# Optimization experiments

Hardware: AMD Instinct MI355X
Metric: run time of the kernel (lower is better)

## Reference

```python
import jax, jax.numpy as jnp
import numpy as np

B, NB, F, N = 8192, 64, 256, 1_000_000
K = 8            # per-channel top-k
KS = K // 2 + 1  # conv1d kernel size = 5
H, OUT = 256, 128
DN = ('NWC', 'WIO', 'NWC')


def setup_inputs() -> dict:
    key = jax.random.key(0)
    ks = jax.random.split(key, 7)
    return {
        'node_ids': jax.random.randint(ks[0], (B,), 0, N, dtype=jnp.int64) if jax.config.jax_enable_x64 else jax.random.randint(ks[0], (B,), 0, N, dtype=jnp.int32),
        'neighbors': jax.random.randint(ks[1], (B, NB), 0, N, dtype=jnp.int32),
        'feat_table': jax.random.normal(ks[2], (N, F), dtype=jnp.float32),
        'W1': jax.random.normal(ks[3], (KS, F, H), dtype=jnp.float32) * 0.05,
        'b1': jnp.zeros((H,), dtype=jnp.float32),
        'W2': jax.random.normal(ks[4], (KS, H, OUT), dtype=jnp.float32) * 0.05,
        'b2': jnp.zeros((OUT,), dtype=jnp.float32),
    }


def reference(node_ids, neighbors, feat_table, W1, b1, W2, b2):
    node_feats = feat_table[node_ids][:, None, :]          # [B, 1, F]
    nb_feats = feat_table[neighbors]                       # [B, NB, F] irregular gather
    # per-channel top-k over neighbors
    topk, _ = jax.lax.top_k(jnp.transpose(nb_feats, (0, 2, 1)), K)  # [B, F, K]
    topk = jnp.transpose(topk, (0, 2, 1))                  # [B, K, F]
    x = jnp.concatenate([node_feats, topk], axis=1)        # [B, K+1, F]
    h = jax.lax.conv_general_dilated(x, W1, (1,), 'VALID', dimension_numbers=DN) + b1  # [B, K+2-KS, H]
    o = jax.lax.conv_general_dilated(h, W2, (1,), 'VALID', dimension_numbers=DN) + b2  # [B, 1, OUT]
    return o[:, 0, :]                                      # [B, OUT]
```

## Files before the change

### kernel.cpp

```cpp
#include <hip/hip_runtime.h>
#include <hip/hip_bf16.h>

namespace {
constexpr int kB    = 8192;
constexpr int kNB   = 64;
constexpr int kF    = 256;
constexpr int kK    = 8;
constexpr int kKS   = 5;
constexpr int kH    = 256;
constexpr int kOUT  = 128;
constexpr int kXR   = 9;
constexpr int kTO   = 5;
constexpr int kBM   = 16;

constexpr int XPAD = 258;
constexpr int HPAD = 1290;

constexpr int DEPTH = 12;

constexpr size_t W1T_OFF = 0;
constexpr size_t W2T_OFF = W1T_OFF + (size_t)kKS * kH * kF * 2;

typedef __attribute__((ext_vector_type(8))) short short8;
typedef __attribute__((ext_vector_type(4))) float f32x4;
}

using bf16 = __hip_bfloat16;

__device__ __forceinline__ unsigned short f2bf(float f) {
  bf16 h = __float2bfloat16(f);
  return *reinterpret_cast<unsigned short*>(&h);
}

__device__ __forceinline__ f32x4 nt_load4(const float* p) {
  return __builtin_nontemporal_load(reinterpret_cast<const f32x4*>(p));
}

__global__ void convert_weights(const float* __restrict__ W1,
                                const float* __restrict__ W2,
                                bf16* __restrict__ w1t, bf16* __restrict__ w2t)
{
  const int i = blockIdx.x * 256 + threadIdx.x;
  const int stride = gridDim.x * 256;
  for (int idx = i; idx < kKS * kH * kF; idx += stride) {
    const int f  = idx & 255;
    const int hc = (idx >> 8) & 255;
    const int dt = idx >> 16;
    w1t[idx] = __float2bfloat16(W1[(dt * kF + f) * kH + hc]);
  }
  for (int idx = i; idx < kOUT * kKS * kH; idx += stride) {
    const int k = idx % (kKS * kH);
    const int o = idx / (kKS * kH);
    w2t[idx] = __float2bfloat16(W2[k * kOUT + o]);
  }
}

__global__ __launch_bounds__(512, 4)
void fused_all(const int* __restrict__ node_ids,
               const int* __restrict__ neighbors,
               const float* __restrict__ feat,
               const bf16* __restrict__ w1t, const bf16* __restrict__ w2t,
               const float* __restrict__ b1, const float* __restrict__ b2,
               float* __restrict__ out)
{
  __shared__ bf16 smem[kBM * kXR * XPAD];
  bf16* xs = smem;
  bf16* hs = smem;

  const int tid  = threadIdx.x;
  const int wave = tid >> 6;
  const int lane = tid & 63;
  const int r = lane & 15;
  const int q = lane >> 4;
  const int bbase = blockIdx.x * kBM;
  const int f4 = lane << 2;

  int   myn2[2];
  f32x4 node2[2];
#pragma unroll
  for (int bb = 0; bb < 2; ++bb) {
    const int b = bbase + wave * 2 + bb;
    myn2[bb]  = neighbors[(size_t)b * kNB + lane];
    node2[bb] = nt_load4(feat + (size_t)node_ids[b] * kF + f4);
  }

#pragma unroll
  for (int bb = 0; bb < 2; ++bb) {
    const int bl  = wave * 2 + bb;
    const int myn = myn2[bb];

    float tk[4][kK];
#pragma unroll
    for (int c = 0; c < 4; ++c)
#pragma unroll
      for (int k = 0; k < kK; ++k) tk[c][k] = -INFINITY;

    auto ins4 = [&](const f32x4& v) {
#pragma unroll
      for (int c = 0; c < 4; ++c) {
        const float vc = v[c];
        float nt[kK];
        nt[0] = fmaxf(tk[c][0], vc);
#pragma unroll
        for (int k = 1; k < kK; ++k)
          nt[k] = __builtin_amdgcn_fmed3f(tk[c][k - 1], tk[c][k], vc);
#pragma unroll
        for (int k = 0; k < kK; ++k) tk[c][k] = nt[k];
      }
    };

    f32x4 buf[DEPTH];
#pragma unroll
    for (int i = 0; i < DEPTH; ++i) {
      const int rr = __builtin_amdgcn_readlane(myn, i);
      buf[i] = nt_load4(feat + (size_t)rr * kF + f4);
    }
#pragma unroll
    for (int n = 0; n < kNB - DEPTH; ++n) {
      const f32x4 v = buf[n % DEPTH];
      const int rr = __builtin_amdgcn_readlane(myn, n + DEPTH);
      buf[n % DEPTH] = nt_load4(feat + (size_t)rr * kF + f4);
      ins4(v);
    }
#pragma unroll
    for (int n = kNB - DEPTH; n < kNB; ++n) ins4(buf[n % DEPTH]);

    bf16* xb = xs + (size_t)bl * kXR * XPAD + f4;
    {
      ushort4 s = {f2bf(node2[bb][0]), f2bf(node2[bb][1]),
                   f2bf(node2[bb][2]), f2bf(node2[bb][3])};
      *reinterpret_cast<ushort4*>(xb) = s;
    }
#pragma unroll
    for (int k = 0; k < kK; ++k) {
      ushort4 s = {f2bf(tk[0][k]), f2bf(tk[1][k]), f2bf(tk[2][k]), f2bf(tk[3][k])};
      *reinterpret_cast<ushort4*>(xb + (size_t)(1 + k) * XPAD) = s;
    }
  }
  __syncthreads();

  const int ntb = wave * 32;
  f32x4 acc[kTO][2];
#pragma unroll
  for (int n = 0; n < 2; ++n) {
    const float bv = b1[ntb + n * 16 + r];
#pragma unroll
    for (int m = 0; m < kTO; ++m) acc[m][n] = (f32x4){bv, bv, bv, bv};
  }

  for (int kk = 0; kk < 8; ++kk) {
    short8 a[kXR];
#pragma unroll
    for (int rr = 0; rr < kXR; ++rr)
      a[rr] = *reinterpret_cast<const short8*>(&xs[(r * kXR + rr) * XPAD + kk * 32 + q * 8]);
#pragma unroll
    for (int dt = 0; dt < kKS; ++dt) {
      short8 bfr[2];
#pragma unroll
      for (int n = 0; n < 2; ++n)
        bfr[n] = *reinterpret_cast<const short8*>(
            &w1t[((size_t)(dt * kH + ntb + n * 16 + r)) * kF + kk * 32 + q * 8]);
#pragma unroll
      for (int m = 0; m < kTO; ++m)
#pragma unroll
        for (int n = 0; n < 2; ++n)
          acc[m][n] = __builtin_amdgcn_mfma_f32_16x16x32_bf16(a[m + dt], bfr[n], acc[m][n], 0, 0, 0);
    }
  }
  __syncthreads();

#pragma unroll
  for (int m = 0; m < kTO; ++m)
#pragma unroll
    for (int n = 0; n < 2; ++n)
#pragma unroll
      for (int j = 0; j < 4; ++j)
        hs[(q * 4 + j) * HPAD + m * kH + ntb + n * 16 + r] = __float2bfloat16(acc[m][n][j]);
  __syncthreads();

  const int ob = wave * 16;
  f32x4 acc2;
  {
    const float bv = b2[ob + r];
    acc2 = (f32x4){bv, bv, bv, bv};
  }
  for (int ks = 0; ks < 40; ++ks) {
    short8 a2 = *reinterpret_cast<const short8*>(&hs[r * HPAD + ks * 32 + q * 8]);
    short8 b2f = *reinterpret_cast<const short8*>(
        &w2t[(size_t)(ob + r) * (kKS * kH) + ks * 32 + q * 8]);
    acc2 = __builtin_amdgcn_mfma_f32_16x16x32_bf16(a2, b2f, acc2, 0, 0, 0);
  }
#pragma unroll
  for (int j = 0; j < 4; ++j)
    out[(size_t)(bbase + q * 4 + j) * kOUT + ob + r] = acc2[j];
}

extern "C" void kernel_launch(void* const* d_in, const int* in_sizes, int n_in,
                              void* d_out, int out_size, void* d_ws, size_t ws_size,
                              hipStream_t stream) {
  const int*   node_ids  = (const int*)  d_in[0];
  const int*   neighbors = (const int*)  d_in[1];
  const float* feat      = (const float*)d_in[2];
  const float* W1        = (const float*)d_in[3];
  const float* b1        = (const float*)d_in[4];
  const float* W2        = (const float*)d_in[5];
  const float* b2        = (const float*)d_in[6];
  float* out = (float*)d_out;

  char* ws = (char*)d_ws;
  bf16* w1t = (bf16*)(ws + W1T_OFF);
  bf16* w2t = (bf16*)(ws + W2T_OFF);

  convert_weights<<<1024, 256, 0, stream>>>(W1, W2, w1t, w2t);
  fused_all<<<kB / kBM, 512, 0, stream>>>(node_ids, neighbors, feat, w1t, w2t, b1, b2, out);
}
```

Baseline: 141.7 us.

## Double batch tile to 32 rows per block and drop nontemporal gather loads

```diff
diff --git a/kernel.cpp b/kernel.cpp
--- a/kernel.cpp
+++ b/kernel.cpp
@@ -11,7 +11,7 @@
 constexpr int kOUT  = 128;
 constexpr int kXR   = 9;
 constexpr int kTO   = 5;
-constexpr int kBM   = 16;
+constexpr int kBM   = 32;
 
 constexpr int XPAD = 258;
 constexpr int HPAD = 1290;
@@ -30,10 +30,6 @@
 __device__ __forceinline__ unsigned short f2bf(float f) {
   bf16 h = __float2bfloat16(f);
   return *reinterpret_cast<unsigned short*>(&h);
-}
-
-__device__ __forceinline__ f32x4 nt_load4(const float* p) {
-  return __builtin_nontemporal_load(reinterpret_cast<const f32x4*>(p));
 }
 
 __global__ void convert_weights(const float* __restrict__ W1,
@@ -55,7 +51,7 @@
   }
 }
 
-__global__ __launch_bounds__(512, 4)
+__global__ __launch_bounds__(512, 2)
 void fused_all(const int* __restrict__ node_ids,
                const int* __restrict__ neighbors,
                const float* __restrict__ feat,
@@ -75,19 +71,19 @@
   const int bbase = blockIdx.x * kBM;
   const int f4 = lane << 2;
 
-  int   myn2[2];
-  f32x4 node2[2];
-#pragma unroll
-  for (int bb = 0; bb < 2; ++bb) {
-    const int b = bbase + wave * 2 + bb;
-    myn2[bb]  = neighbors[(size_t)b * kNB + lane];
-    node2[bb] = nt_load4(feat + (size_t)node_ids[b] * kF + f4);
-  }
-
-#pragma unroll
-  for (int bb = 0; bb < 2; ++bb) {
-    const int bl  = wave * 2 + bb;
-    const int myn = myn2[bb];
+  int   myn4[4];
+  f32x4 node4[4];
+#pragma unroll
+  for (int bb = 0; bb < 4; ++bb) {
+    const int b = bbase + wave * 4 + bb;
+    myn4[bb]  = neighbors[(size_t)b * kNB + lane];
+    node4[bb] = *reinterpret_cast<const f32x4*>(feat + (size_t)node_ids[b] * kF + f4);
+  }
+
+#pragma unroll
+  for (int bb = 0; bb < 4; ++bb) {
+    const int bl  = wave * 4 + bb;
+    const int myn = myn4[bb];
 
     float tk[4][kK];
 #pragma unroll
@@ -113,13 +109,13 @@
 #pragma unroll
     for (int i = 0; i < DEPTH; ++i) {
       const int rr = __builtin_amdgcn_readlane(myn, i);
-      buf[i] = nt_load4(feat + (size_t)rr * kF + f4);
+      buf[i] = *reinterpret_cast<const f32x4*>(feat + (size_t)rr * kF + f4);
     }
 #pragma unroll
     for (int n = 0; n < kNB - DEPTH; ++n) {
       const f32x4 v = buf[n % DEPTH];
       const int rr = __builtin_amdgcn_readlane(myn, n + DEPTH);
-      buf[n % DEPTH] = nt_load4(feat + (size_t)rr * kF + f4);
+      buf[n % DEPTH] = *reinterpret_cast<const f32x4*>(feat + (size_t)rr * kF + f4);
       ins4(v);
     }
 #pragma unroll
@@ -127,8 +123,8 @@
 
     bf16* xb = xs + (size_t)bl * kXR * XPAD + f4;
     {
-      ushort4 s = {f2bf(node2[bb][0]), f2bf(node2[bb][1]),
-                   f2bf(node2[bb][2]), f2bf(node2[bb][3])};
+      ushort4 s = {f2bf(node4[bb][0]), f2bf(node4[bb][1]),
+                   f2bf(node4[bb][2]), f2bf(node4[bb][3])};
       *reinterpret_cast<ushort4*>(xb) = s;
     }
 #pragma unroll
@@ -140,19 +136,24 @@
   __syncthreads();
 
   const int ntb = wave * 32;
-  f32x4 acc[kTO][2];
+  f32x4 acc[2][kTO][2];
 #pragma unroll
   for (int n = 0; n < 2; ++n) {
     const float bv = b1[ntb + n * 16 + r];
 #pragma unroll
-    for (int m = 0; m < kTO; ++m) acc[m][n] = (f32x4){bv, bv, bv, bv};
+    for (int mt = 0; mt < 2; ++mt)
+#pragma unroll
+      for (int m = 0; m < kTO; ++m) acc[mt][m][n] = (f32x4){bv, bv, bv, bv};
   }
 
   for (int kk = 0; kk < 8; ++kk) {
-    short8 a[kXR];
-#pragma unroll
-    for (int rr = 0; rr < kXR; ++rr)
-      a[rr] = *reinterpret_cast<const short8*>(&xs[(r * kXR + rr) * XPAD + kk * 32 + q * 8]);
+    short8 a[2][kXR];
+#pragma unroll
+    for (int mt = 0; mt < 2; ++mt)
+#pragma unroll
+      for (int rr = 0; rr < kXR; ++rr)
+        a[mt][rr] = *reinterpret_cast<const short8*>(
+            &xs[((mt * 16 + r) * kXR + rr) * XPAD + kk * 32 + q * 8]);
 #pragma unroll
     for (int dt = 0; dt < kKS; ++dt) {
       short8 bfr[2];
@@ -161,38 +162,51 @@
         bfr[n] = *reinterpret_cast<const short8*>(
             &w1t[((size_t)(dt * kH + ntb + n * 16 + r)) * kF + kk * 32 + q * 8]);
 #pragma unroll
-      for (int m = 0; m < kTO; ++m)
-#pragma unroll
-        for (int n = 0; n < 2; ++n)
-          acc[m][n] = __builtin_amdgcn_mfma_f32_16x16x32_bf16(a[m + dt], bfr[n], acc[m][n], 0, 0, 0);
+      for (int mt = 0; mt < 2; ++mt)
+#pragma unroll
+        for (int m = 0; m < kTO; ++m)
+#pragma unroll
+          for (int n = 0; n < 2; ++n)
+            acc[mt][m][n] = __builtin_amdgcn_mfma_f32_16x16x32_bf16(
+                a[mt][m + dt], bfr[n], acc[mt][m][n], 0, 0, 0);
     }
   }
   __syncthreads();
 
 #pragma unroll
-  for (int m = 0; m < kTO; ++m)
-#pragma unroll
-    for (int n = 0; n < 2; ++n)
-#pragma unroll
-      for (int j = 0; j < 4; ++j)
-        hs[(q * 4 + j) * HPAD + m * kH + ntb + n * 16 + r] = __float2bfloat16(acc[m][n][j]);
+  for (int mt = 0; mt < 2; ++mt)
+#pragma unroll
+    for (int m = 0; m < kTO; ++m)
+#pragma unroll
+      for (int n = 0; n < 2; ++n)
+#pragma unroll
+        for (int j = 0; j < 4; ++j)
+          hs[(mt * 16 + q * 4 + j) * HPAD + m * kH + ntb + n * 16 + r] =
+              __float2bfloat16(acc[mt][m][n][j]);
   __syncthreads();
 
   const int ob = wave * 16;
-  f32x4 acc2;
+  f32x4 acc2[2];
   {
     const float bv = b2[ob + r];
-    acc2 = (f32x4){bv, bv, bv, bv};
+#pragma unroll
+    for (int mt = 0; mt < 2; ++mt) acc2[mt] = (f32x4){bv, bv, bv, bv};
   }
   for (int ks = 0; ks < 40; ++ks) {
-    short8 a2 = *reinterpret_cast<const short8*>(&hs[r * HPAD + ks * 32 + q * 8]);
     short8 b2f = *reinterpret_cast<const short8*>(
         &w2t[(size_t)(ob + r) * (kKS * kH) + ks * 32 + q * 8]);
-    acc2 = __builtin_amdgcn_mfma_f32_16x16x32_bf16(a2, b2f, acc2, 0, 0, 0);
-  }
-#pragma unroll
-  for (int j = 0; j < 4; ++j)
-    out[(size_t)(bbase + q * 4 + j) * kOUT + ob + r] = acc2[j];
+#pragma unroll
+    for (int mt = 0; mt < 2; ++mt) {
+      short8 a2 = *reinterpret_cast<const short8*>(
+          &hs[(mt * 16 + r) * HPAD + ks * 32 + q * 8]);
+      acc2[mt] = __builtin_amdgcn_mfma_f32_16x16x32_bf16(a2, b2f, acc2[mt], 0, 0, 0);
+    }
+  }
+#pragma unroll
+  for (int mt = 0; mt < 2; ++mt)
+#pragma unroll
+    for (int j = 0; j < 4; ++j)
+      out[(size_t)(bbase + mt * 16 + q * 4 + j) * kOUT + ob + r] = acc2[mt][j];
 }
 
 extern "C" void kernel_launch(void* const* d_in, const int* in_sizes, int n_in,
```

Result: no change. 144.5 us (+1.9%).

## Process two tiles per block, overlapping next tile's gather with current GEMMs

Applied to the files above, without the earlier changes.

```diff
diff --git a/kernel.cpp b/kernel.cpp
--- a/kernel.cpp
+++ b/kernel.cpp
@@ -12,11 +12,10 @@
 constexpr int kXR   = 9;
 constexpr int kTO   = 5;
 constexpr int kBM   = 16;
+constexpr int kTiles = 2;
 
 constexpr int XPAD = 258;
 constexpr int HPAD = 1290;
-
-constexpr int DEPTH = 12;
 
 constexpr size_t W1T_OFF = 0;
 constexpr size_t W2T_OFF = W1T_OFF + (size_t)kKS * kH * kF * 2;
@@ -32,8 +31,54 @@
   return *reinterpret_cast<unsigned short*>(&h);
 }
 
-__device__ __forceinline__ f32x4 nt_load4(const float* p) {
-  return __builtin_nontemporal_load(reinterpret_cast<const f32x4*>(p));
+__device__ __forceinline__ void ins4(const f32x4& v, float (&tk)[4][kK]) {
+#pragma unroll
+  for (int c = 0; c < 4; ++c) {
+    const float vc = v[c];
+    float nt[kK];
+    nt[0] = fmaxf(tk[c][0], vc);
+#pragma unroll
+    for (int k = 1; k < kK; ++k)
+      nt[k] = __builtin_amdgcn_fmed3f(tk[c][k - 1], tk[c][k], vc);
+#pragma unroll
+    for (int k = 0; k < kK; ++k) tk[c][k] = nt[k];
+  }
+}
+
+__device__ __forceinline__ f32x4 rowload(const float* feat, int myn, int idx, int f4) {
+  const unsigned rr = (unsigned)__builtin_amdgcn_readlane(myn, idx);
+  return *reinterpret_cast<const f32x4*>(feat + (size_t)rr * kF + f4);
+}
+
+__device__ __forceinline__ void store_x(bf16* xb, const f32x4& nodev, float (&tk)[4][kK]) {
+  ushort4 s0 = {f2bf(nodev[0]), f2bf(nodev[1]), f2bf(nodev[2]), f2bf(nodev[3])};
+  *reinterpret_cast<ushort4*>(xb) = s0;
+#pragma unroll
+  for (int k = 0; k < kK; ++k) {
+    ushort4 s = {f2bf(tk[0][k]), f2bf(tk[1][k]), f2bf(tk[2][k]), f2bf(tk[3][k])};
+    *reinterpret_cast<ushort4*>(xb + (size_t)(1 + k) * XPAD) = s;
+  }
+}
+
+__device__ __forceinline__ void gather_row(const float* feat, int myn, int f4,
+                                           const f32x4& nodev, bf16* xb) {
+  float tk[4][kK];
+#pragma unroll
+  for (int c = 0; c < 4; ++c)
+#pragma unroll
+    for (int k = 0; k < kK; ++k) tk[c][k] = -INFINITY;
+  f32x4 buf[8];
+#pragma unroll
+  for (int i = 0; i < 8; ++i) buf[i] = rowload(feat, myn, i, f4);
+#pragma unroll
+  for (int g = 0; g < 8; ++g)
+#pragma unroll
+    for (int i = 0; i < 8; ++i) {
+      const f32x4 v = buf[i];
+      if (g < 7) buf[i] = rowload(feat, myn, g * 8 + i + 8, f4);
+      ins4(v, tk);
+    }
+  store_x(xb, nodev, tk);
 }
 
 __global__ void convert_weights(const float* __restrict__ W1,
@@ -55,7 +100,7 @@
   }
 }
 
-__global__ __launch_bounds__(512, 4)
+__global__ __launch_bounds__(512, 2)
 void fused_all(const int* __restrict__ node_ids,
                const int* __restrict__ neighbors,
                const float* __restrict__ feat,
@@ -63,83 +108,53 @@
                const float* __restrict__ b1, const float* __restrict__ b2,
                float* __restrict__ out)
 {
-  __shared__ bf16 smem[kBM * kXR * XPAD];
-  bf16* xs = smem;
-  bf16* hs = smem;
+  __shared__ bf16 smem[2 * kBM * kXR * XPAD];
+  bf16* xsA = smem;
+  bf16* xsB = smem + (size_t)kBM * kXR * XPAD;
+  bf16* hs  = smem;
 
   const int tid  = threadIdx.x;
   const int wave = tid >> 6;
   const int lane = tid & 63;
   const int r = lane & 15;
   const int q = lane >> 4;
-  const int bbase = blockIdx.x * kBM;
   const int f4 = lane << 2;
 
-  int   myn2[2];
-  f32x4 node2[2];
-#pragma unroll
-  for (int bb = 0; bb < 2; ++bb) {
-    const int b = bbase + wave * 2 + bb;
-    myn2[bb]  = neighbors[(size_t)b * kNB + lane];
-    node2[bb] = nt_load4(feat + (size_t)node_ids[b] * kF + f4);
-  }
-
-#pragma unroll
-  for (int bb = 0; bb < 2; ++bb) {
-    const int bl  = wave * 2 + bb;
-    const int myn = myn2[bb];
-
-    float tk[4][kK];
-#pragma unroll
-    for (int c = 0; c < 4; ++c)
-#pragma unroll
-      for (int k = 0; k < kK; ++k) tk[c][k] = -INFINITY;
-
-    auto ins4 = [&](const f32x4& v) {
-#pragma unroll
-      for (int c = 0; c < 4; ++c) {
-        const float vc = v[c];
-        float nt[kK];
-        nt[0] = fmaxf(tk[c][0], vc);
-#pragma unroll
-        for (int k = 1; k < kK; ++k)
-          nt[k] = __builtin_amdgcn_fmed3f(tk[c][k - 1], tk[c][k], vc);
-#pragma unroll
-        for (int k = 0; k < kK; ++k) tk[c][k] = nt[k];
-      }
-    };
-
-    f32x4 buf[DEPTH];
-#pragma unroll
-    for (int i = 0; i < DEPTH; ++i) {
-      const int rr = __builtin_amdgcn_readlane(myn, i);
-      buf[i] = nt_load4(feat + (size_t)rr * kF + f4);
-    }
-#pragma unroll
-    for (int n = 0; n < kNB - DEPTH; ++n) {
-      const f32x4 v = buf[n % DEPTH];
-      const int rr = __builtin_amdgcn_readlane(myn, n + DEPTH);
-      buf[n % DEPTH] = nt_load4(feat + (size_t)rr * kF + f4);
-      ins4(v);
-    }
-#pragma unroll
-    for (int n = kNB - DEPTH; n < kNB; ++n) ins4(buf[n % DEPTH]);
-
-    bf16* xb = xs + (size_t)bl * kXR * XPAD + f4;
-    {
-      ushort4 s = {f2bf(node2[bb][0]), f2bf(node2[bb][1]),
-                   f2bf(node2[bb][2]), f2bf(node2[bb][3])};
-      *reinterpret_cast<ushort4*>(xb) = s;
-    }
-#pragma unroll
-    for (int k = 0; k < kK; ++k) {
-      ushort4 s = {f2bf(tk[0][k]), f2bf(tk[1][k]), f2bf(tk[2][k]), f2bf(tk[3][k])};
-      *reinterpret_cast<ushort4*>(xb + (size_t)(1 + k) * XPAD) = s;
-    }
-  }
-  __syncthreads();
+  const int tile0 = blockIdx.x;
+  const int tile1 = blockIdx.x + 256;
+  const int bbase0 = tile0 * kBM;
+  const int bbase1 = tile1 * kBM;
+
+  {
+    int   mynA[2];
+    f32x4 nodeA[2];
+#pragma unroll
+    for (int bb = 0; bb < 2; ++bb) {
+      const int b = bbase0 + wave * 2 + bb;
+      mynA[bb]  = neighbors[(size_t)b * kNB + lane];
+      nodeA[bb] = *reinterpret_cast<const f32x4*>(feat + (size_t)node_ids[b] * kF + f4);
+    }
+#pragma unroll
+    for (int bb = 0; bb < 2; ++bb)
+      gather_row(feat, mynA[bb], f4, nodeA[bb],
+                 xsA + (size_t)(wave * 2 + bb) * kXR * XPAD + f4);
+  }
+  __syncthreads();
+
+  int   mynB0, mynB1;
+  f32x4 nodeB0, nodeB1;
+  {
+    const int b0 = bbase1 + wave * 2 + 0;
+    const int b1r = bbase1 + wave * 2 + 1;
+    mynB0  = neighbors[(size_t)b0 * kNB + lane];
+    mynB1  = neighbors[(size_t)b1r * kNB + lane];
+    nodeB0 = *reinterpret_cast<const f32x4*>(feat + (size_t)node_ids[b0] * kF + f4);
+    nodeB1 = *reinterpret_cast<const f32x4*>(feat + (size_t)node_ids[b1r] * kF + f4);
+  }
 
   const int ntb = wave * 32;
+  const int ob  = wave * 16;
+
   f32x4 acc[kTO][2];
 #pragma unroll
   for (int n = 0; n < 2; ++n) {
@@ -148,11 +163,103 @@
     for (int m = 0; m < kTO; ++m) acc[m][n] = (f32x4){bv, bv, bv, bv};
   }
 
+  {
+    float tkB[4][kK];
+#pragma unroll
+    for (int c = 0; c < 4; ++c)
+#pragma unroll
+      for (int k = 0; k < kK; ++k) tkB[c][k] = -INFINITY;
+    f32x4 bufB[8];
+#pragma unroll
+    for (int i = 0; i < 8; ++i) bufB[i] = rowload(feat, mynB0, i, f4);
+
+    for (int kk = 0; kk < 8; ++kk) {
+#pragma unroll
+      for (int i = 0; i < 8; ++i) {
+        const f32x4 v = bufB[i];
+        if (kk < 7) bufB[i] = rowload(feat, mynB0, kk * 8 + i + 8, f4);
+        ins4(v, tkB);
+      }
+      short8 a[kXR];
+#pragma unroll
+      for (int rr = 0; rr < kXR; ++rr)
+        a[rr] = *reinterpret_cast<const short8*>(&xsA[(r * kXR + rr) * XPAD + kk * 32 + q * 8]);
+#pragma unroll
+      for (int dt = 0; dt < kKS; ++dt) {
+        short8 bfr[2];
+#pragma unroll
+        for (int n = 0; n < 2; ++n)
+          bfr[n] = *reinterpret_cast<const short8*>(
+              &w1t[((size_t)(dt * kH + ntb + n * 16 + r)) * kF + kk * 32 + q * 8]);
+#pragma unroll
+        for (int m = 0; m < kTO; ++m)
+#pragma unroll
+          for (int n = 0; n < 2; ++n)
+            acc[m][n] = __builtin_amdgcn_mfma_f32_16x16x32_bf16(a[m + dt], bfr[n], acc[m][n], 0, 0, 0);
+      }
+    }
+    store_x(xsB + (size_t)(wave * 2 + 0) * kXR * XPAD + f4, nodeB0, tkB);
+  }
+  __syncthreads();
+
+#pragma unroll
+  for (int m = 0; m < kTO; ++m)
+#pragma unroll
+    for (int n = 0; n < 2; ++n)
+#pragma unroll
+      for (int j = 0; j < 4; ++j)
+        hs[(q * 4 + j) * HPAD + m * kH + ntb + n * 16 + r] = __float2bfloat16(acc[m][n][j]);
+  __syncthreads();
+
+  {
+    float tkB[4][kK];
+#pragma unroll
+    for (int c = 0; c < 4; ++c)
+#pragma unroll
+      for (int k = 0; k < kK; ++k) tkB[c][k] = -INFINITY;
+    f32x4 bufB[8];
+#pragma unroll
+    for (int i = 0; i < 8; ++i) bufB[i] = rowload(feat, mynB1, i, f4);
+
+    f32x4 acc2;
+    {
+      const float bv = b2[ob + r];
+      acc2 = (f32x4){bv, bv, bv, bv};
+    }
+    for (int c = 0; c < 8; ++c) {
+#pragma unroll
+      for (int i = 0; i < 8; ++i) {
+        const f32x4 v = bufB[i];
+        if (c < 7) bufB[i] = rowload(feat, mynB1, c * 8 + i + 8, f4);
+        ins4(v, tkB);
+      }
+#pragma unroll
+      for (int j = 0; j < 5; ++j) {
+        const int ks = c * 5 + j;
+        short8 a2 = *reinterpret_cast<const short8*>(&hs[r * HPAD + ks * 32 + q * 8]);
+        short8 b2f = *reinterpret_cast<const short8*>(
+            &w2t[(size_t)(ob + r) * (kKS * kH) + ks * 32 + q * 8]);
+        acc2 = __builtin_amdgcn_mfma_f32_16x16x32_bf16(a2, b2f, acc2, 0, 0, 0);
+      }
+    }
+#pragma unroll
+    for (int j = 0; j < 4; ++j)
+      out[(size_t)(bbase0 + q * 4 + j) * kOUT + ob + r] = acc2[j];
+    store_x(xsB + (size_t)(wave * 2 + 1) * kXR * XPAD + f4, nodeB1, tkB);
+  }
+  __syncthreads();
+
+#pragma unroll
+  for (int n = 0; n < 2; ++n) {
+    const float bv = b1[ntb + n * 16 + r];
+#pragma unroll
+    for (int m = 0; m < kTO; ++m) acc[m][n] = (f32x4){bv, bv, bv, bv};
+  }
   for (int kk = 0; kk < 8; ++kk) {
     short8 a[kXR];
 #pragma unroll
     for (int rr = 0; rr < kXR; ++rr)
-      a[rr] = *reinterpret_cast<const short8*>(&xs[(r * kXR + rr) * XPAD + kk * 32 + q * 8]);
+      a[rr] = *reinterpret_cast<const short8*>(&xsB[(r * kXR + rr) * XPAD + kk * 32 + q * 8]);
 #pragma unroll
     for (int dt = 0; dt < kKS; ++dt) {
       short8 bfr[2];
@@ -178,21 +285,20 @@
         hs[(q * 4 + j) * HPAD + m * kH + ntb + n * 16 + r] = __float2bfloat16(acc[m][n][j]);
   __syncthreads();
 
-  const int ob = wave * 16;
-  f32x4 acc2;
-  {
+  {
+    f32x4 acc2;
     const float bv = b2[ob + r];
     acc2 = (f32x4){bv, bv, bv, bv};
-  }
-  for (int ks = 0; ks < 40; ++ks) {
-    short8 a2 = *reinterpret_cast<const short8*>(&hs[r * HPAD + ks * 32 + q * 8]);
-    short8 b2f = *reinterpret_cast<const short8*>(
-        &w2t[(size_t)(ob + r) * (kKS * kH) + ks * 32 + q * 8]);
-    acc2 = __builtin_amdgcn_mfma_f32_16x16x32_bf16(a2, b2f, acc2, 0, 0, 0);
-  }
-#pragma unroll
-  for (int j = 0; j < 4; ++j)
-    out[(size_t)(bbase + q * 4 + j) * kOUT + ob + r] = acc2[j];
+    for (int ks = 0; ks < 40; ++ks) {
+      short8 a2 = *reinterpret_cast<const short8*>(&hs[r * HPAD + ks * 32 + q * 8]);
+      short8 b2f = *reinterpret_cast<const short8*>(
+          &w2t[(size_t)(ob + r) * (kKS * kH) + ks * 32 + q * 8]);
+      acc2 = __builtin_amdgcn_mfma_f32_16x16x32_bf16(a2, b2f, acc2, 0, 0, 0);
+    }
+#pragma unroll
+    for (int j = 0; j < 4; ++j)
+      out[(size_t)(bbase1 + q * 4 + j) * kOUT + ob + r] = acc2[j];
+  }
 }
 
 extern "C" void kernel_launch(void* const* d_in, const int* in_sizes, int n_in,
@@ -212,5 +318,6 @@
   bf16* w2t = (bf16*)(ws + W2T_OFF);
 
   convert_weights<<<1024, 256, 0, stream>>>(W1, W2, w1t, w2t);
-  fused_all<<<kB / kBM, 512, 0, stream>>>(node_ids, neighbors, feat, w1t, w2t, b1, b2, out);
-}
+  fused_all<<<kB / (kBM * kTiles), 512, 0, stream>>>(node_ids, neighbors, feat,
+                                                     w1t, w2t, b1, b2, out);
+}
```

Result: no change. 144.0 us (+1.6%).
